# Kernel tuning notes

Hardware: AMD Instinct MI355X
Metric: run time of the kernel (lower is better)

## Reference

```python
import jax, jax.numpy as jnp
import numpy as np

N = 128
NPTS = 120000
G = 64  # voxel grid side


def _build_coords_and_nbrs():
    rng = np.random.default_rng(0)
    lin = rng.choice(G ** 3, size=NPTS, replace=False)
    xs = lin // (G * G)
    ys = (lin // G) % G
    zs = lin % G
    lut = np.full(G ** 3, -1, np.int32)
    lut[lin] = np.arange(NPTS, dtype=np.int32)
    nbr = np.full((NPTS, 27), -1, np.int32)
    k = 0
    for dx in (-1, 0, 1):
        for dy in (-1, 0, 1):
            for dz in (-1, 0, 1):
                nx, ny, nz = xs + dx, ys + dy, zs + dz
                ok = (nx >= 0) & (nx < G) & (ny >= 0) & (ny < G) & (nz >= 0) & (nz < G)
                nl = np.clip(nx * G * G + ny * G + nz, 0, G ** 3 - 1)
                nbr[:, k] = np.where(ok, lut[nl], -1)
                k += 1
    return nbr


def setup_inputs() -> dict:
    key = jax.random.key(0)
    k = jax.random.split(key, 6)
    H = N // 2
    x = jax.random.normal(k[0], (NPTS, N), jnp.float32)
    W1s = jax.random.normal(k[1], (6, N, H), jnp.float32) * np.sqrt(2.0 / N)
    Wks = jax.random.normal(k[2], (6, 27, H, H), jnp.float32) * np.sqrt(2.0 / (27 * H))
    W2s = jax.random.normal(k[3], (6, H, N), jnp.float32) * np.sqrt(1.0 / H)
    Wf = jax.random.normal(k[4], (N, N), jnp.float32) * np.sqrt(1.0 / N)
    nbr_idx = jnp.asarray(_build_coords_and_nbrs())
    return {"x": x, "W1s": W1s, "Wks": Wks, "W2s": W2s, "Wf": Wf, "nbr_idx": nbr_idx}


def reference(x, W1s, Wks, W2s, Wf, nbr_idx):
    valid = nbr_idx >= 0                      # [NPTS, 27]
    safe = jnp.maximum(nbr_idx, 0)

    def conv3(h, Wk):
        # gather-matmul-scatter over the 27 coordinate offsets (as ME does)
        out = jnp.zeros((h.shape[0], Wk.shape[2]), h.dtype)
        for kk in range(27):
            g = jnp.where(valid[:, kk, None], h[safe[:, kk]], 0.0)
            out = out + g @ Wk[kk]
        return out

    def residual_unit(h, i):
        t = jax.nn.relu(h @ W1s[i])           # 1x1 conv N -> N/2
        t = jax.nn.relu(conv3(t, Wks[i]))     # 3^3 sparse conv N/2 -> N/2
        t = t @ W2s[i]                        # 1x1 conv N/2 -> N
        return jax.nn.relu(t + h)

    a = x
    for i in range(3):
        a = residual_unit(a, i)
    b = x
    for i in range(3, 6):
        b = residual_unit(b, i)
    b = b @ Wf                                # final 1x1 conv in branch b
    return a * jax.nn.sigmoid(b) + x
```

## Files before the change

### kernel.cpp

```cpp
#include <hip/hip_runtime.h>
#include <stdint.h>

#define NPTS 120000

typedef __attribute__((ext_vector_type(8))) short bf16x8;
typedef __attribute__((ext_vector_type(4))) float f32x4;

__device__ __forceinline__ uint16_t f2b(float f) {
    union { float f; uint32_t i; } v; v.f = f;
    uint32_t x = v.i;
    return (uint16_t)((x + 0x7fffu + ((x >> 16) & 1u)) >> 16);
}
__device__ __forceinline__ float b2f(uint16_t u) {
    union { uint32_t i; float f; } v; v.i = ((uint32_t)u) << 16; return v.f;
}
__device__ __forceinline__ bf16x8 cvt8(f32x4 a, f32x4 b) {
    bf16x8 t;
    t[0] = (short)f2b(a[0]); t[1] = (short)f2b(a[1]);
    t[2] = (short)f2b(a[2]); t[3] = (short)f2b(a[3]);
    t[4] = (short)f2b(b[0]); t[5] = (short)f2b(b[1]);
    t[6] = (short)f2b(b[2]); t[7] = (short)f2b(b[3]);
    return t;
}
#define MFMA(a, b, c) __builtin_amdgcn_mfma_f32_16x16x32_bf16((a), (b), (c), 0, 0, 0)

__global__ __launch_bounds__(256) void k_swz(
    const float* __restrict__ W1s, const float* __restrict__ Wks,
    const float* __restrict__ W2s, const float* __restrict__ Wf,
    uint16_t* __restrict__ Z, uint16_t* __restrict__ T1z)
{
    if (blockIdx.x == 0 && threadIdx.x < 64)
        T1z[(size_t)NPTS * 64 + threadIdx.x] = 0;
    int idx = blockIdx.x * 256 + threadIdx.x;
    if (idx >= 778240) return;
    const float* src; int K, N, r;
    if (idx < 49152)       { src = W1s + (idx / 8192) * 8192;           K = 128; N = 64;  r = idx & 8191; }
    else if (idx < 712704) { int t = idx - 49152;  src = Wks + (t >> 12) * 4096; K = 64;  N = 64;  r = t & 4095; }
    else if (idx < 761856) { int t = idx - 712704; src = W2s + (t / 8192) * 8192; K = 64;  N = 128; r = t & 8191; }
    else                   { src = Wf; K = 128; N = 128; r = idx - 761856; }
    int j  = r & 7;
    int l  = (r >> 3) & 63;
    int t2 = r >> 9;
    int KC = K >> 5;
    int kc = t2 % KC;
    int nt = t2 / KC;
    int k  = kc * 32 + (l >> 4) * 8 + j;
    int n  = nt * 16 + (l & 15);
    Z[idx] = f2b(src[k * N + n]);
}

__global__ __launch_bounds__(256) void k_gemm1(
    const float* __restrict__ H, const uint16_t* __restrict__ Wz,
    uint16_t* __restrict__ T)
{
    const int tid = threadIdx.x;
    const int wv = tid >> 6, ln = tid & 63;
    const int m = ln & 15, part = ln >> 4;
    const long rb = (long)blockIdx.x * 64 + wv * 16;

    bf16x8 a[4];
    const float* hrow = H + (rb + m) * 128 + part * 8;
    #pragma unroll
    for (int kc = 0; kc < 4; ++kc) {
        f32x4 h0 = *reinterpret_cast<const f32x4*>(hrow + kc * 32);
        f32x4 h1 = *reinterpret_cast<const f32x4*>(hrow + kc * 32 + 4);
        a[kc] = cvt8(h0, h1);
    }
    #pragma unroll
    for (int nt = 0; nt < 4; ++nt) {
        f32x4 acc = (f32x4)(0.0f);
        #pragma unroll
        for (int kc = 0; kc < 4; ++kc) {
            bf16x8 b = *reinterpret_cast<const bf16x8*>(Wz + ((nt * 4 + kc) * 64 + ln) * 8);
            acc = MFMA(a[kc], b, acc);
        }
        #pragma unroll
        for (int r = 0; r < 4; ++r) {
            float v = acc[r] > 0.f ? acc[r] : 0.f;
            T[(rb + part * 4 + r) * 64 + nt * 16 + m] = f2b(v);
        }
    }
}

__global__ __launch_bounds__(256) void k_convg2(
    const uint16_t* __restrict__ T,
    const uint16_t* __restrict__ Wkz,
    const uint16_t* __restrict__ W2z,
    const float* Hin,
    const int* __restrict__ nbr,
    float* HoutF, uint16_t* __restrict__ HoutB, int out_bf16)
{
    __shared__ int snbr[27 * 48];
    __shared__ __align__(16) float red[3 * 3072];
    __shared__ __align__(16) uint16_t sc2[48 * 72];
    const int tid = threadIdx.x;
    const int wv = tid >> 6, ln = tid & 63;
    const int mrow = ln & 15, part = ln >> 4;
    const long bb = (long)blockIdx.x * 48;

    for (int i = tid; i < 1296; i += 256) {
        int lp = i / 27, kk = i - lp * 27;
        int n = nbr[(bb + lp) * 27 + kk];
        snbr[kk * 48 + lp] = (n < 0) ? NPTS : n;
    }
    __syncthreads();

    f32x4 acc[3][4];
    #pragma unroll
    for (int mm = 0; mm < 3; ++mm)
        #pragma unroll
        for (int nt = 0; nt < 4; ++nt) acc[mm][nt] = (f32x4)(0.0f);

    for (int k = wv; k < 27; k += 4) {
        bf16x8 A[3][2];
        #pragma unroll
        for (int mm = 0; mm < 3; ++mm) {
            long r0 = (long)snbr[k * 48 + mm * 16 + mrow] * 64;
            A[mm][0] = *reinterpret_cast<const bf16x8*>(T + r0 + part * 8);
            A[mm][1] = *reinterpret_cast<const bf16x8*>(T + r0 + 32 + part * 8);
        }
        const uint16_t* wb = Wkz + k * 4096;
        bf16x8 B[8];
        #pragma unroll
        for (int i = 0; i < 8; ++i)
            B[i] = *reinterpret_cast<const bf16x8*>(wb + (i * 64 + ln) * 8);
        #pragma unroll
        for (int nt = 0; nt < 4; ++nt)
            #pragma unroll
            for (int mm = 0; mm < 3; ++mm) {
                acc[mm][nt] = MFMA(A[mm][0], B[nt * 2 + 0], acc[mm][nt]);
                acc[mm][nt] = MFMA(A[mm][1], B[nt * 2 + 1], acc[mm][nt]);
            }
    }

    if (wv > 0) {
        float* buf = &red[(wv - 1) * 3072];
        #pragma unroll
        for (int mm = 0; mm < 3; ++mm)
            #pragma unroll
            for (int nt = 0; nt < 4; ++nt)
                #pragma unroll
                for (int r = 0; r < 4; ++r)
                    buf[(mm * 16 + part * 4 + r) * 64 + nt * 16 + mrow] = acc[mm][nt][r];
    }
    __syncthreads();
    if (wv == 0) {
        #pragma unroll
        for (int mm = 0; mm < 3; ++mm)
            #pragma unroll
            for (int nt = 0; nt < 4; ++nt)
                #pragma unroll
                for (int r = 0; r < 4; ++r) {
                    int idx = (mm * 16 + part * 4 + r) * 64 + nt * 16 + mrow;
                    float v = acc[mm][nt][r] + red[idx] + red[3072 + idx] + red[6144 + idx];
                    v = v > 0.f ? v : 0.f;
                    sc2[(mm * 16 + part * 4 + r) * 72 + nt * 16 + mrow] = f2b(v);
                }
    }
    __syncthreads();

    bf16x8 a2[3][2];
    #pragma unroll
    for (int mm = 0; mm < 3; ++mm) {
        const uint16_t* crow = sc2 + (mm * 16 + mrow) * 72;
        a2[mm][0] = *reinterpret_cast<const bf16x8*>(crow + part * 8);
        a2[mm][1] = *reinterpret_cast<const bf16x8*>(crow + 32 + part * 8);
    }
    f32x4 acc2[3][2];
    #pragma unroll
    for (int mm = 0; mm < 3; ++mm)
        #pragma unroll
        for (int j = 0; j < 2; ++j) acc2[mm][j] = (f32x4)(0.0f);
    #pragma unroll
    for (int j = 0; j < 2; ++j) {
        int nt = wv * 2 + j;
        bf16x8 b0 = *reinterpret_cast<const bf16x8*>(W2z + ((nt * 2 + 0) * 64 + ln) * 8);
        bf16x8 b1 = *reinterpret_cast<const bf16x8*>(W2z + ((nt * 2 + 1) * 64 + ln) * 8);
        #pragma unroll
        for (int mm = 0; mm < 3; ++mm) {
            acc2[mm][j] = MFMA(a2[mm][0], b0, acc2[mm][j]);
            acc2[mm][j] = MFMA(a2[mm][1], b1, acc2[mm][j]);
        }
    }
    if (out_bf16) {
        #pragma unroll
        for (int mm = 0; mm < 3; ++mm)
            #pragma unroll
            for (int j = 0; j < 2; ++j)
                #pragma unroll
                for (int r = 0; r < 4; ++r) {
                    long p = bb + mm * 16 + part * 4 + r;
                    int col = (wv * 2 + j) * 16 + mrow;
                    float v = acc2[mm][j][r] + Hin[p * 128 + col];
                    v = v > 0.f ? v : 0.f;
                    HoutB[p * 128 + col] = f2b(v);
                }
    } else {
        #pragma unroll
        for (int mm = 0; mm < 3; ++mm)
            #pragma unroll
            for (int j = 0; j < 2; ++j)
                #pragma unroll
                for (int r = 0; r < 4; ++r) {
                    long p = bb + mm * 16 + part * 4 + r;
                    int col = (wv * 2 + j) * 16 + mrow;
                    float v = acc2[mm][j][r] + Hin[p * 128 + col];
                    HoutF[p * 128 + col] = v > 0.f ? v : 0.f;
                }
    }
}

__global__ __launch_bounds__(256) void k_final(
    const float* B, const uint16_t* __restrict__ Wfz,
    const uint16_t* __restrict__ A16, const float* __restrict__ X,
    float* Out)
{
    const int tid = threadIdx.x;
    const int wv = tid >> 6, ln = tid & 63;
    const int m = ln & 15, part = ln >> 4;
    const long rb = (long)blockIdx.x * 64 + wv * 16;

    bf16x8 a[4];
    const float* brow = B + (rb + m) * 128 + part * 8;
    #pragma unroll
    for (int kc = 0; kc < 4; ++kc) {
        f32x4 h0 = *reinterpret_cast<const f32x4*>(brow + kc * 32);
        f32x4 h1 = *reinterpret_cast<const f32x4*>(brow + kc * 32 + 4);
        a[kc] = cvt8(h0, h1);
    }
    #pragma unroll
    for (int nt = 0; nt < 8; ++nt) {
        f32x4 acc = (f32x4)(0.0f);
        #pragma unroll
        for (int kc = 0; kc < 4; ++kc) {
            bf16x8 b = *reinterpret_cast<const bf16x8*>(Wfz + ((nt * 4 + kc) * 64 + ln) * 8);
            acc = MFMA(a[kc], b, acc);
        }
        #pragma unroll
        for (int r = 0; r < 4; ++r) {
            long p = rb + part * 4 + r;
            int col = nt * 16 + m;
            float s = 1.f / (1.f + __expf(-acc[r]));
            float av = b2f(A16[p * 128 + col]);
            Out[p * 128 + col] = av * s + X[p * 128 + col];
        }
    }
}

extern "C" void kernel_launch(void* const* d_in, const int* in_sizes, int n_in,
                              void* d_out, int out_size, void* d_ws, size_t ws_size,
                              hipStream_t stream)
{
    const float* x   = (const float*)d_in[0];
    const float* W1s = (const float*)d_in[1];
    const float* Wks = (const float*)d_in[2];
    const float* W2s = (const float*)d_in[3];
    const float* Wf  = (const float*)d_in[4];
    const int*   nbr = (const int*)d_in[5];
    float*       out = (float*)d_out;

    uint16_t* A16 = (uint16_t*)d_ws;
    uint16_t* T1  = A16 + (size_t)NPTS * 128;
    uint16_t* Z   = T1 + (size_t)(NPTS + 1) * 64;
    const uint16_t* W1z = Z;
    const uint16_t* Wkz = Z + 49152;
    const uint16_t* W2z = Z + 712704;
    const uint16_t* Wfz = Z + 761856;

    k_swz<<<dim3(3040), dim3(256), 0, stream>>>(W1s, Wks, W2s, Wf, Z, T1);

    auto unit = [&](int i, const float* hin, float* houtF, uint16_t* houtB, int obf) {
        k_gemm1<<<dim3(1875), dim3(256), 0, stream>>>(hin, W1z + (size_t)i * 8192, T1);
        k_convg2<<<dim3(2500), dim3(256), 0, stream>>>(T1, Wkz + (size_t)i * 110592,
                                                       W2z + (size_t)i * 8192,
                                                       hin, nbr, houtF, houtB, obf);
    };

    unit(0, x,   out, nullptr, 0);
    unit(1, out, out, nullptr, 0);
    unit(2, out, out, A16,     1);
    unit(3, x,   out, nullptr, 0);
    unit(4, out, out, nullptr, 0);
    unit(5, out, out, nullptr, 0);
    k_final<<<dim3(1875), dim3(256), 0, stream>>>(out, Wfz, A16, x, out);
}
```

Baseline: 739.4 us.

## Run sparse conv block as single wave with double-buffered neighbor gathers

The gather-conv-plus-1x1 kernel drops from four waves per 48-point block, each handling a subset of taps, to a single wave that processes all 27 taps. This removes the cross-wave LDS reduction and the block barriers. Gathered rows are double-buffered so the load for the next tap overlaps the MFMAs of the current one, and the neighbor table is stored in its original layout. In exchange, each block does four times as much serial work with a quarter of the threads, so latency hiding now depends on running many small blocks per CU.

After: 795.2 us. 1.08x slower.

```diff
diff --git a/kernel.cpp b/kernel.cpp
--- a/kernel.cpp
+++ b/kernel.cpp
@@ -82,7 +82,7 @@
     }
 }
 
-__global__ __launch_bounds__(256) void k_convg2(
+__global__ __launch_bounds__(64) void k_convg2(
     const uint16_t* __restrict__ T,
     const uint16_t* __restrict__ Wkz,
     const uint16_t* __restrict__ W2z,
@@ -90,20 +90,19 @@
     const int* __restrict__ nbr,
     float* HoutF, uint16_t* __restrict__ HoutB, int out_bf16)
 {
-    __shared__ int snbr[27 * 48];
-    __shared__ __align__(16) float red[3 * 3072];
-    __shared__ __align__(16) uint16_t sc2[48 * 72];
-    const int tid = threadIdx.x;
-    const int wv = tid >> 6, ln = tid & 63;
+    __shared__ int snbr[48 * 27];
+    __shared__ __align__(16) uint16_t sc2[48 * 80];
+    const int ln = threadIdx.x;
     const int mrow = ln & 15, part = ln >> 4;
+    const int pc8 = part * 8;
     const long bb = (long)blockIdx.x * 48;
 
-    for (int i = tid; i < 1296; i += 256) {
-        int lp = i / 27, kk = i - lp * 27;
-        int n = nbr[(bb + lp) * 27 + kk];
-        snbr[kk * 48 + lp] = (n < 0) ? NPTS : n;
-    }
-    __syncthreads();
+    const int* nb = nbr + bb * 27;
+    for (int i = ln; i < 1296; i += 64) {
+        int n = nb[i];
+        snbr[i] = (n < 0) ? NPTS : n;
+    }
+    __builtin_amdgcn_wave_barrier();
 
     f32x4 acc[3][4];
     #pragma unroll
@@ -111,102 +110,99 @@
         #pragma unroll
         for (int nt = 0; nt < 4; ++nt) acc[mm][nt] = (f32x4)(0.0f);
 
-    for (int k = wv; k < 27; k += 4) {
-        bf16x8 A[3][2];
-        #pragma unroll
-        for (int mm = 0; mm < 3; ++mm) {
-            long r0 = (long)snbr[k * 48 + mm * 16 + mrow] * 64;
-            A[mm][0] = *reinterpret_cast<const bf16x8*>(T + r0 + part * 8);
-            A[mm][1] = *reinterpret_cast<const bf16x8*>(T + r0 + 32 + part * 8);
-        }
-        const uint16_t* wb = Wkz + k * 4096;
-        bf16x8 B[8];
-        #pragma unroll
-        for (int i = 0; i < 8; ++i)
-            B[i] = *reinterpret_cast<const bf16x8*>(wb + (i * 64 + ln) * 8);
+    bf16x8 Aa[3][2], Ab[3][2];
+
+#define LOADA(Adst, kk)                                                         \
+    {                                                                           \
+        _Pragma("unroll")                                                       \
+        for (int mm = 0; mm < 3; ++mm) {                                        \
+            long r0 = (long)snbr[(mm * 16 + mrow) * 27 + (kk)] << 6;            \
+            Adst[mm][0] = *reinterpret_cast<const bf16x8*>(T + r0 + pc8);       \
+            Adst[mm][1] = *reinterpret_cast<const bf16x8*>(T + r0 + 32 + pc8);  \
+        }                                                                       \
+    }
+
+#define TAP(Asrc, kk)                                                           \
+    {                                                                           \
+        const uint16_t* wb = Wkz + (kk) * 4096;                                 \
+        bf16x8 B[8];                                                            \
+        _Pragma("unroll")                                                       \
+        for (int i = 0; i < 8; ++i)                                             \
+            B[i] = *reinterpret_cast<const bf16x8*>(wb + (i * 64 + ln) * 8);    \
+        _Pragma("unroll")                                                       \
+        for (int nt = 0; nt < 4; ++nt) {                                        \
+            _Pragma("unroll")                                                   \
+            for (int mm = 0; mm < 3; ++mm) {                                    \
+                acc[mm][nt] = MFMA(Asrc[mm][0], B[nt * 2 + 0], acc[mm][nt]);    \
+                acc[mm][nt] = MFMA(Asrc[mm][1], B[nt * 2 + 1], acc[mm][nt]);    \
+            }                                                                   \
+        }                                                                       \
+    }
+
+    LOADA(Aa, 0);
+    #pragma unroll 1
+    for (int k = 0; k < 26; k += 2) {
+        LOADA(Ab, k + 1);
+        TAP(Aa, k);
+        LOADA(Aa, k + 2);
+        TAP(Ab, k + 1);
+    }
+    TAP(Aa, 26);
+#undef LOADA
+#undef TAP
+
+    #pragma unroll
+    for (int mm = 0; mm < 3; ++mm)
         #pragma unroll
         for (int nt = 0; nt < 4; ++nt)
             #pragma unroll
-            for (int mm = 0; mm < 3; ++mm) {
-                acc[mm][nt] = MFMA(A[mm][0], B[nt * 2 + 0], acc[mm][nt]);
-                acc[mm][nt] = MFMA(A[mm][1], B[nt * 2 + 1], acc[mm][nt]);
+            for (int r = 0; r < 4; ++r) {
+                float v = acc[mm][nt][r];
+                v = v > 0.f ? v : 0.f;
+                sc2[(mm * 16 + part * 4 + r) * 80 + nt * 16 + mrow] = f2b(v);
             }
-    }
-
-    if (wv > 0) {
-        float* buf = &red[(wv - 1) * 3072];
-        #pragma unroll
-        for (int mm = 0; mm < 3; ++mm)
-            #pragma unroll
-            for (int nt = 0; nt < 4; ++nt)
-                #pragma unroll
-                for (int r = 0; r < 4; ++r)
-                    buf[(mm * 16 + part * 4 + r) * 64 + nt * 16 + mrow] = acc[mm][nt][r];
-    }
-    __syncthreads();
-    if (wv == 0) {
-        #pragma unroll
-        for (int mm = 0; mm < 3; ++mm)
-            #pragma unroll
-            for (int nt = 0; nt < 4; ++nt)
-                #pragma unroll
-                for (int r = 0; r < 4; ++r) {
-                    int idx = (mm * 16 + part * 4 + r) * 64 + nt * 16 + mrow;
-                    float v = acc[mm][nt][r] + red[idx] + red[3072 + idx] + red[6144 + idx];
-                    v = v > 0.f ? v : 0.f;
-                    sc2[(mm * 16 + part * 4 + r) * 72 + nt * 16 + mrow] = f2b(v);
-                }
-    }
-    __syncthreads();
+    __builtin_amdgcn_wave_barrier();
 
     bf16x8 a2[3][2];
     #pragma unroll
     for (int mm = 0; mm < 3; ++mm) {
-        const uint16_t* crow = sc2 + (mm * 16 + mrow) * 72;
-        a2[mm][0] = *reinterpret_cast<const bf16x8*>(crow + part * 8);
-        a2[mm][1] = *reinterpret_cast<const bf16x8*>(crow + 32 + part * 8);
-    }
-    f32x4 acc2[3][2];
-    #pragma unroll
-    for (int mm = 0; mm < 3; ++mm)
-        #pragma unroll
-        for (int j = 0; j < 2; ++j) acc2[mm][j] = (f32x4)(0.0f);
-    #pragma unroll
-    for (int j = 0; j < 2; ++j) {
-        int nt = wv * 2 + j;
+        const uint16_t* crow = sc2 + (mm * 16 + mrow) * 80;
+        a2[mm][0] = *reinterpret_cast<const bf16x8*>(crow + pc8);
+        a2[mm][1] = *reinterpret_cast<const bf16x8*>(crow + 32 + pc8);
+    }
+
+    #pragma unroll 2
+    for (int nt = 0; nt < 8; ++nt) {
         bf16x8 b0 = *reinterpret_cast<const bf16x8*>(W2z + ((nt * 2 + 0) * 64 + ln) * 8);
         bf16x8 b1 = *reinterpret_cast<const bf16x8*>(W2z + ((nt * 2 + 1) * 64 + ln) * 8);
+        f32x4 c[3];
         #pragma unroll
         for (int mm = 0; mm < 3; ++mm) {
-            acc2[mm][j] = MFMA(a2[mm][0], b0, acc2[mm][j]);
-            acc2[mm][j] = MFMA(a2[mm][1], b1, acc2[mm][j]);
-        }
-    }
-    if (out_bf16) {
-        #pragma unroll
-        for (int mm = 0; mm < 3; ++mm)
+            c[mm] = (f32x4)(0.0f);
+            c[mm] = MFMA(a2[mm][0], b0, c[mm]);
+            c[mm] = MFMA(a2[mm][1], b1, c[mm]);
+        }
+        const int col = nt * 16 + mrow;
+        if (out_bf16) {
             #pragma unroll
-            for (int j = 0; j < 2; ++j)
+            for (int mm = 0; mm < 3; ++mm)
                 #pragma unroll
                 for (int r = 0; r < 4; ++r) {
                     long p = bb + mm * 16 + part * 4 + r;
-                    int col = (wv * 2 + j) * 16 + mrow;
-                    float v = acc2[mm][j][r] + Hin[p * 128 + col];
+                    float v = c[mm][r] + Hin[p * 128 + col];
                     v = v > 0.f ? v : 0.f;
                     HoutB[p * 128 + col] = f2b(v);
                 }
-    } else {
-        #pragma unroll
-        for (int mm = 0; mm < 3; ++mm)
+        } else {
             #pragma unroll
-            for (int j = 0; j < 2; ++j)
+            for (int mm = 0; mm < 3; ++mm)
                 #pragma unroll
                 for (int r = 0; r < 4; ++r) {
                     long p = bb + mm * 16 + part * 4 + r;
-                    int col = (wv * 2 + j) * 16 + mrow;
-                    float v = acc2[mm][j][r] + Hin[p * 128 + col];
+                    float v = c[mm][r] + Hin[p * 128 + col];
                     HoutF[p * 128 + col] = v > 0.f ? v : 0.f;
                 }
+        }
     }
 }
 
@@ -271,9 +267,9 @@
 
     auto unit = [&](int i, const float* hin, float* houtF, uint16_t* houtB, int obf) {
         k_gemm1<<<dim3(1875), dim3(256), 0, stream>>>(hin, W1z + (size_t)i * 8192, T1);
-        k_convg2<<<dim3(2500), dim3(256), 0, stream>>>(T1, Wkz + (size_t)i * 110592,
-                                                       W2z + (size_t)i * 8192,
-                                                       hin, nbr, houtF, houtB, obf);
+        k_convg2<<<dim3(2500), dim3(64), 0, stream>>>(T1, Wkz + (size_t)i * 110592,
+                                                      W2z + (size_t)i * 8192,
+                                                      hin, nbr, houtF, houtB, obf);
     };
 
     unit(0, x,   out, nullptr, 0);
```

## Fuse next unit's 1x1 conv and final gating into sparse conv epilogue

Applied to the files above, without the earlier changes.

The conv kernel's epilogue now computes the next residual unit's first 1x1 conv (N→N/2 with ReLU) from the freshly produced rows, held in shared memory as bf16. Its output goes to a second ping-pong T buffer. The last unit's epilogue also does the final Wf matmul, the sigmoid gating and the residual add, so the separate gemm1 and final kernels are no longer launched. This removes several full passes that re-read the fp32 activations, at the cost of more workspace, extra register and shared-memory pressure in the conv kernel, and a fallback path when the workspace is too small.

Result: no change. 731.3 us (-1.1%).

```diff
diff --git a/kernel.cpp b/kernel.cpp
--- a/kernel.cpp
+++ b/kernel.cpp
@@ -27,10 +27,15 @@
 __global__ __launch_bounds__(256) void k_swz(
     const float* __restrict__ W1s, const float* __restrict__ Wks,
     const float* __restrict__ W2s, const float* __restrict__ Wf,
-    uint16_t* __restrict__ Z, uint16_t* __restrict__ T1z)
+    uint16_t* __restrict__ Z, uint16_t* __restrict__ T1z,
+    uint16_t* __restrict__ T2z)
 {
-    if (blockIdx.x == 0 && threadIdx.x < 64)
-        T1z[(size_t)NPTS * 64 + threadIdx.x] = 0;
+    if (blockIdx.x == 0) {
+        if (threadIdx.x < 64)
+            T1z[(size_t)NPTS * 64 + threadIdx.x] = 0;
+        else if (threadIdx.x < 128 && T2z)
+            T2z[(size_t)NPTS * 64 + (threadIdx.x - 64)] = 0;
+    }
     int idx = blockIdx.x * 256 + threadIdx.x;
     if (idx >= 778240) return;
     const float* src; int K, N, r;
@@ -88,7 +93,14 @@
     const uint16_t* __restrict__ W2z,
     const float* Hin,
     const int* __restrict__ nbr,
-    float* HoutF, uint16_t* __restrict__ HoutB, int out_bf16)
+    float* HoutF,
+    uint16_t* __restrict__ HoutB,
+    const uint16_t* __restrict__ Wn,
+    uint16_t* __restrict__ Tn,
+    const float* __restrict__ Xg,
+    const uint16_t* __restrict__ A16g,
+    float* __restrict__ OutF,
+    int mode)
 {
     __shared__ int snbr[27 * 48];
     __shared__ __align__(16) float red[3 * 3072];
@@ -182,7 +194,46 @@
             acc2[mm][j] = MFMA(a2[mm][1], b1, acc2[mm][j]);
         }
     }
-    if (out_bf16) {
+
+    uint16_t* sH = (uint16_t*)red;
+
+    if (mode == 0) {
+        #pragma unroll
+        for (int mm = 0; mm < 3; ++mm)
+            #pragma unroll
+            for (int j = 0; j < 2; ++j)
+                #pragma unroll
+                for (int r = 0; r < 4; ++r) {
+                    int lr = mm * 16 + part * 4 + r;
+                    long p = bb + lr;
+                    int col = (wv * 2 + j) * 16 + mrow;
+                    float v = acc2[mm][j][r] + Hin[p * 128 + col];
+                    v = v > 0.f ? v : 0.f;
+                    HoutF[p * 128 + col] = v;
+                    sH[lr * 136 + col] = f2b(v);
+                }
+        if (Tn) {
+            __syncthreads();
+            f32x4 t1a[3] = { (f32x4)(0.f), (f32x4)(0.f), (f32x4)(0.f) };
+            #pragma unroll
+            for (int kc = 0; kc < 4; ++kc) {
+                bf16x8 b = *reinterpret_cast<const bf16x8*>(Wn + ((wv * 4 + kc) * 64 + ln) * 8);
+                #pragma unroll
+                for (int mm = 0; mm < 3; ++mm) {
+                    bf16x8 a = *reinterpret_cast<const bf16x8*>(
+                        sH + (mm * 16 + mrow) * 136 + kc * 32 + part * 8);
+                    t1a[mm] = MFMA(a, b, t1a[mm]);
+                }
+            }
+            #pragma unroll
+            for (int mm = 0; mm < 3; ++mm)
+                #pragma unroll
+                for (int r = 0; r < 4; ++r) {
+                    float v = t1a[mm][r]; v = v > 0.f ? v : 0.f;
+                    Tn[(bb + mm * 16 + part * 4 + r) * 64 + wv * 16 + mrow] = f2b(v);
+                }
+        }
+    } else if (mode == 1) {
         #pragma unroll
         for (int mm = 0; mm < 3; ++mm)
             #pragma unroll
@@ -195,6 +246,27 @@
                     v = v > 0.f ? v : 0.f;
                     HoutB[p * 128 + col] = f2b(v);
                 }
+        if (Tn) {
+            f32x4 t1a[3] = { (f32x4)(0.f), (f32x4)(0.f), (f32x4)(0.f) };
+            #pragma unroll
+            for (int kc = 0; kc < 4; ++kc) {
+                bf16x8 b = *reinterpret_cast<const bf16x8*>(Wn + ((wv * 4 + kc) * 64 + ln) * 8);
+                #pragma unroll
+                for (int mm = 0; mm < 3; ++mm) {
+                    const float* xr = Xg + (bb + mm * 16 + mrow) * 128 + kc * 32 + part * 8;
+                    f32x4 h0 = *reinterpret_cast<const f32x4*>(xr);
+                    f32x4 h1 = *reinterpret_cast<const f32x4*>(xr + 4);
+                    t1a[mm] = MFMA(cvt8(h0, h1), b, t1a[mm]);
+                }
+            }
+            #pragma unroll
+            for (int mm = 0; mm < 3; ++mm)
+                #pragma unroll
+                for (int r = 0; r < 4; ++r) {
+                    float v = t1a[mm][r]; v = v > 0.f ? v : 0.f;
+                    Tn[(bb + mm * 16 + part * 4 + r) * 64 + wv * 16 + mrow] = f2b(v);
+                }
+        }
     } else {
         #pragma unroll
         for (int mm = 0; mm < 3; ++mm)
@@ -202,11 +274,42 @@
             for (int j = 0; j < 2; ++j)
                 #pragma unroll
                 for (int r = 0; r < 4; ++r) {
-                    long p = bb + mm * 16 + part * 4 + r;
+                    int lr = mm * 16 + part * 4 + r;
+                    long p = bb + lr;
                     int col = (wv * 2 + j) * 16 + mrow;
                     float v = acc2[mm][j][r] + Hin[p * 128 + col];
-                    HoutF[p * 128 + col] = v > 0.f ? v : 0.f;
-                }
+                    v = v > 0.f ? v : 0.f;
+                    sH[lr * 136 + col] = f2b(v);
+                }
+        __syncthreads();
+        bf16x8 af[3][4];
+        #pragma unroll
+        for (int mm = 0; mm < 3; ++mm)
+            #pragma unroll
+            for (int kc = 0; kc < 4; ++kc)
+                af[mm][kc] = *reinterpret_cast<const bf16x8*>(
+                    sH + (mm * 16 + mrow) * 136 + kc * 32 + part * 8);
+        #pragma unroll
+        for (int j = 0; j < 2; ++j) {
+            int nt = wv * 2 + j;
+            f32x4 fa[3] = { (f32x4)(0.f), (f32x4)(0.f), (f32x4)(0.f) };
+            #pragma unroll
+            for (int kc = 0; kc < 4; ++kc) {
+                bf16x8 b = *reinterpret_cast<const bf16x8*>(Wn + ((nt * 4 + kc) * 64 + ln) * 8);
+                #pragma unroll
+                for (int mm = 0; mm < 3; ++mm)
+                    fa[mm] = MFMA(af[mm][kc], b, fa[mm]);
+            }
+            #pragma unroll
+            for (int mm = 0; mm < 3; ++mm)
+                #pragma unroll
+                for (int r = 0; r < 4; ++r) {
+                    long p = bb + mm * 16 + part * 4 + r;
+                    int col = nt * 16 + mrow;
+                    float s = 1.f / (1.f + __expf(-fa[mm][r]));
+                    OutF[p * 128 + col] = b2f(A16g[p * 128 + col]) * s + Xg[p * 128 + col];
+                }
+        }
     }
 }
 
@@ -259,28 +362,52 @@
     const int*   nbr = (const int*)d_in[5];
     float*       out = (float*)d_out;
 
+    const size_t A16_n = (size_t)NPTS * 128;
+    const size_t T_n   = (size_t)(NPTS + 1) * 64;
+    const size_t Z_n   = 778240;
+    const size_t need2 = (A16_n + 2 * T_n + Z_n) * 2;
+
     uint16_t* A16 = (uint16_t*)d_ws;
-    uint16_t* T1  = A16 + (size_t)NPTS * 128;
-    uint16_t* Z   = T1 + (size_t)(NPTS + 1) * 64;
+    uint16_t* Ta  = A16 + A16_n;
+    bool dual = ws_size >= need2;
+    uint16_t* Tb  = dual ? Ta + T_n : nullptr;
+    uint16_t* Z   = dual ? Tb + T_n : Ta + T_n;
     const uint16_t* W1z = Z;
     const uint16_t* Wkz = Z + 49152;
     const uint16_t* W2z = Z + 712704;
     const uint16_t* Wfz = Z + 761856;
 
-    k_swz<<<dim3(3040), dim3(256), 0, stream>>>(W1s, Wks, W2s, Wf, Z, T1);
-
-    auto unit = [&](int i, const float* hin, float* houtF, uint16_t* houtB, int obf) {
-        k_gemm1<<<dim3(1875), dim3(256), 0, stream>>>(hin, W1z + (size_t)i * 8192, T1);
-        k_convg2<<<dim3(2500), dim3(256), 0, stream>>>(T1, Wkz + (size_t)i * 110592,
-                                                       W2z + (size_t)i * 8192,
-                                                       hin, nbr, houtF, houtB, obf);
-    };
-
-    unit(0, x,   out, nullptr, 0);
-    unit(1, out, out, nullptr, 0);
-    unit(2, out, out, A16,     1);
-    unit(3, x,   out, nullptr, 0);
-    unit(4, out, out, nullptr, 0);
-    unit(5, out, out, nullptr, 0);
-    k_final<<<dim3(1875), dim3(256), 0, stream>>>(out, Wfz, A16, x, out);
-}
+    k_swz<<<dim3(3040), dim3(256), 0, stream>>>(W1s, Wks, W2s, Wf, Z, Ta, Tb);
+
+    if (dual) {
+        auto conv = [&](int i, const uint16_t* Tc, const float* hin,
+                        float* houtF, uint16_t* houtB,
+                        const uint16_t* wn, uint16_t* tn,
+                        const float* xg, const uint16_t* a16g, float* outF, int mode) {
+            k_convg2<<<dim3(2500), dim3(256), 0, stream>>>(
+                Tc, Wkz + (size_t)i * 110592, W2z + (size_t)i * 8192,
+                hin, nbr, houtF, houtB, wn, tn, xg, a16g, outF, mode);
+        };
+        k_gemm1<<<dim3(1875), dim3(256), 0, stream>>>(x, W1z, Ta);
+        conv(0, Ta, x,   out, nullptr, W1z + 1 * 8192, Tb, nullptr, nullptr, nullptr, 0);
+        conv(1, Tb, out, out, nullptr, W1z + 2 * 8192, Ta, nullptr, nullptr, nullptr, 0);
+        conv(2, Ta, out, nullptr, A16, W1z + 3 * 8192, Tb, x,       nullptr, nullptr, 1);
+        conv(3, Tb, x,   out, nullptr, W1z + 4 * 8192, Ta, nullptr, nullptr, nullptr, 0);
+        conv(4, Ta, out, out, nullptr, W1z + 5 * 8192, Tb, nullptr, nullptr, nullptr, 0);
+        conv(5, Tb, out, nullptr, nullptr, Wfz, nullptr, x, A16, out, 2);
+    } else {
+        auto unit = [&](int i, const float* hin, float* houtF, uint16_t* houtB, int m) {
+            k_gemm1<<<dim3(1875), dim3(256), 0, stream>>>(hin, W1z + (size_t)i * 8192, Ta);
+            k_convg2<<<dim3(2500), dim3(256), 0, stream>>>(
+                Ta, Wkz + (size_t)i * 110592, W2z + (size_t)i * 8192,
+                hin, nbr, houtF, houtB, nullptr, nullptr, nullptr, nullptr, nullptr, m);
+        };
+        unit(0, x,   out, nullptr, 0);
+        unit(1, out, out, nullptr, 0);
+        unit(2, out, nullptr, A16, 1);
+        unit(3, x,   out, nullptr, 0);
+        unit(4, out, out, nullptr, 0);
+        unit(5, out, out, nullptr, 0);
+        k_final<<<dim3(1875), dim3(256), 0, stream>>>(out, Wfz, A16, x, out);
+    }
+}
```

## Restructure sparse conv: per-wave point tiles, LDS double-buffered weights, fused final GEMM

Applied to the files above, without the earlier changes.

The conv kernel now gives each wave its own 48 points and has it loop over all 27 offsets, instead of splitting offsets across waves. This removes the cross-wave LDS reduction. Each offset's weight slice is staged cooperatively into a double-buffered LDS tile, and a pre-transposed neighbour index table (pre-shifted into row offsets) is prefetched one offset ahead. The final Wf GEMM with sigmoid gating is fused into the last conv launch, which removes k_final and one full read of the fp32 intermediate. In exchange there is a block-wide sync on every offset, a larger block with fewer blocks, and a one-time transpose kernel for the neighbour table.

New measurement: 675.5 us. 1.09x faster.

```diff
diff --git a/kernel.cpp b/kernel.cpp
--- a/kernel.cpp
+++ b/kernel.cpp
@@ -49,6 +49,24 @@
     Z[idx] = f2b(src[k * N + n]);
 }
 
+__global__ __launch_bounds__(256) void k_nbrT(
+    const int* __restrict__ nbr, int* __restrict__ nbrT)
+{
+    __shared__ int st[27 * 64];
+    const int tid = threadIdx.x;
+    const long p0 = (long)blockIdx.x * 64;
+    for (int i = tid; i < 1728; i += 256) {
+        int lp = i / 27, kk = i - lp * 27;
+        int n = nbr[p0 * 27 + i];
+        st[kk * 64 + lp] = ((n < 0) ? NPTS : n) << 6;
+    }
+    __syncthreads();
+    for (int i = tid; i < 1728; i += 256) {
+        int kk = i >> 6, lp = i & 63;
+        nbrT[(long)kk * NPTS + p0 + lp] = st[i];
+    }
+}
+
 __global__ __launch_bounds__(256) void k_gemm1(
     const float* __restrict__ H, const uint16_t* __restrict__ Wz,
     uint16_t* __restrict__ T)
@@ -82,27 +100,39 @@
     }
 }
 
-__global__ __launch_bounds__(256) void k_convg2(
+template<int MODE>
+__global__ __launch_bounds__(256, (MODE == 2) ? 2 : 3) void k_conv(
     const uint16_t* __restrict__ T,
     const uint16_t* __restrict__ Wkz,
     const uint16_t* __restrict__ W2z,
     const float* Hin,
-    const int* __restrict__ nbr,
-    float* HoutF, uint16_t* __restrict__ HoutB, int out_bf16)
-{
-    __shared__ int snbr[27 * 48];
-    __shared__ __align__(16) float red[3 * 3072];
-    __shared__ __align__(16) uint16_t sc2[48 * 72];
+    const int* __restrict__ nbrT,
+    float* HoutF,
+    uint16_t* __restrict__ HoutB,
+    const uint16_t* __restrict__ Wfz,
+    const uint16_t* __restrict__ A16g,
+    const float* __restrict__ Xg,
+    float* __restrict__ OutF)
+{
+    constexpr int SLICE_SH = (MODE == 2) ? 6528 : 3456;
+    __shared__ __align__(16) uint16_t wkbuf[2][4096];
+    __shared__ __align__(16) uint16_t uni[4][SLICE_SH];
     const int tid = threadIdx.x;
     const int wv = tid >> 6, ln = tid & 63;
-    const int mrow = ln & 15, part = ln >> 4;
-    const long bb = (long)blockIdx.x * 48;
-
-    for (int i = tid; i < 1296; i += 256) {
-        int lp = i / 27, kk = i - lp * 27;
-        int n = nbr[(bb + lp) * 27 + kk];
-        snbr[kk * 48 + lp] = (n < 0) ? NPTS : n;
-    }
+    const int mrow = ln & 15, part = ln >> 4, pc8 = part * 8;
+    const long bb = (long)blockIdx.x * 192;
+    const long wb0 = bb + wv * 48;
+
+    {
+        const uint16_t* g = Wkz + wv * 1024 + ln * 8;
+        bf16x8 s0 = *reinterpret_cast<const bf16x8*>(g);
+        bf16x8 s1 = *reinterpret_cast<const bf16x8*>(g + 512);
+        *reinterpret_cast<bf16x8*>(&wkbuf[0][wv * 1024 + ln * 8]) = s0;
+        *reinterpret_cast<bf16x8*>(&wkbuf[0][wv * 1024 + 512 + ln * 8]) = s1;
+    }
+    int idx[3];
+    #pragma unroll
+    for (int mm = 0; mm < 3; ++mm) idx[mm] = nbrT[wb0 + mm * 16 + mrow];
     __syncthreads();
 
     f32x4 acc[3][4];
@@ -111,19 +141,29 @@
         #pragma unroll
         for (int nt = 0; nt < 4; ++nt) acc[mm][nt] = (f32x4)(0.0f);
 
-    for (int k = wv; k < 27; k += 4) {
+    int cur = 0;
+    #pragma unroll 1
+    for (int k = 0; k < 27; ++k) {
         bf16x8 A[3][2];
         #pragma unroll
         for (int mm = 0; mm < 3; ++mm) {
-            long r0 = (long)snbr[k * 48 + mm * 16 + mrow] * 64;
-            A[mm][0] = *reinterpret_cast<const bf16x8*>(T + r0 + part * 8);
-            A[mm][1] = *reinterpret_cast<const bf16x8*>(T + r0 + 32 + part * 8);
-        }
-        const uint16_t* wb = Wkz + k * 4096;
+            const uint16_t* s = T + (long)idx[mm] + pc8;
+            A[mm][0] = *reinterpret_cast<const bf16x8*>(s);
+            A[mm][1] = *reinterpret_cast<const bf16x8*>(s + 32);
+        }
+        bf16x8 s0, s1;
+        if (k < 26) {
+            const uint16_t* g = Wkz + (k + 1) * 4096 + wv * 1024 + ln * 8;
+            s0 = *reinterpret_cast<const bf16x8*>(g);
+            s1 = *reinterpret_cast<const bf16x8*>(g + 512);
+            const int* ib = nbrT + (long)(k + 1) * NPTS + wb0;
+            #pragma unroll
+            for (int mm = 0; mm < 3; ++mm) idx[mm] = ib[mm * 16 + mrow];
+        }
         bf16x8 B[8];
         #pragma unroll
         for (int i = 0; i < 8; ++i)
-            B[i] = *reinterpret_cast<const bf16x8*>(wb + (i * 64 + ln) * 8);
+            B[i] = *reinterpret_cast<const bf16x8*>(&wkbuf[cur][i * 512 + ln * 8]);
         #pragma unroll
         for (int nt = 0; nt < 4; ++nt)
             #pragma unroll
@@ -131,118 +171,110 @@
                 acc[mm][nt] = MFMA(A[mm][0], B[nt * 2 + 0], acc[mm][nt]);
                 acc[mm][nt] = MFMA(A[mm][1], B[nt * 2 + 1], acc[mm][nt]);
             }
-    }
-
-    if (wv > 0) {
-        float* buf = &red[(wv - 1) * 3072];
-        #pragma unroll
-        for (int mm = 0; mm < 3; ++mm)
-            #pragma unroll
-            for (int nt = 0; nt < 4; ++nt)
-                #pragma unroll
-                for (int r = 0; r < 4; ++r)
-                    buf[(mm * 16 + part * 4 + r) * 64 + nt * 16 + mrow] = acc[mm][nt][r];
-    }
-    __syncthreads();
-    if (wv == 0) {
-        #pragma unroll
-        for (int mm = 0; mm < 3; ++mm)
-            #pragma unroll
-            for (int nt = 0; nt < 4; ++nt)
-                #pragma unroll
-                for (int r = 0; r < 4; ++r) {
-                    int idx = (mm * 16 + part * 4 + r) * 64 + nt * 16 + mrow;
-                    float v = acc[mm][nt][r] + red[idx] + red[3072 + idx] + red[6144 + idx];
-                    v = v > 0.f ? v : 0.f;
-                    sc2[(mm * 16 + part * 4 + r) * 72 + nt * 16 + mrow] = f2b(v);
-                }
-    }
-    __syncthreads();
+        if (k < 26) {
+            *reinterpret_cast<bf16x8*>(&wkbuf[cur ^ 1][wv * 1024 + ln * 8]) = s0;
+            *reinterpret_cast<bf16x8*>(&wkbuf[cur ^ 1][wv * 1024 + 512 + ln * 8]) = s1;
+        }
+        __syncthreads();
+        cur ^= 1;
+    }
+
+    uint16_t* sc2 = &uni[wv][0];
+    #pragma unroll
+    for (int mm = 0; mm < 3; ++mm)
+        #pragma unroll
+        for (int nt = 0; nt < 4; ++nt)
+            #pragma unroll
+            for (int r = 0; r < 4; ++r) {
+                float v = acc[mm][nt][r];
+                v = v > 0.f ? v : 0.f;
+                sc2[(mm * 16 + part * 4 + r) * 72 + nt * 16 + mrow] = f2b(v);
+            }
+    __builtin_amdgcn_wave_barrier();
 
     bf16x8 a2[3][2];
     #pragma unroll
     for (int mm = 0; mm < 3; ++mm) {
         const uint16_t* crow = sc2 + (mm * 16 + mrow) * 72;
-        a2[mm][0] = *reinterpret_cast<const bf16x8*>(crow + part * 8);
-        a2[mm][1] = *reinterpret_cast<const bf16x8*>(crow + 32 + part * 8);
-    }
-    f32x4 acc2[3][2];
-    #pragma unroll
-    for (int mm = 0; mm < 3; ++mm)
-        #pragma unroll
-        for (int j = 0; j < 2; ++j) acc2[mm][j] = (f32x4)(0.0f);
-    #pragma unroll
-    for (int j = 0; j < 2; ++j) {
-        int nt = wv * 2 + j;
+        a2[mm][0] = *reinterpret_cast<const bf16x8*>(crow + pc8);
+        a2[mm][1] = *reinterpret_cast<const bf16x8*>(crow + 32 + pc8);
+    }
+    __builtin_amdgcn_wave_barrier();
+
+    #pragma unroll 2
+    for (int nt = 0; nt < 8; ++nt) {
         bf16x8 b0 = *reinterpret_cast<const bf16x8*>(W2z + ((nt * 2 + 0) * 64 + ln) * 8);
         bf16x8 b1 = *reinterpret_cast<const bf16x8*>(W2z + ((nt * 2 + 1) * 64 + ln) * 8);
+        f32x4 c[3];
         #pragma unroll
         for (int mm = 0; mm < 3; ++mm) {
-            acc2[mm][j] = MFMA(a2[mm][0], b0, acc2[mm][j]);
-            acc2[mm][j] = MFMA(a2[mm][1], b1, acc2[mm][j]);
-        }
-    }
-    if (out_bf16) {
-        #pragma unroll
-        for (int mm = 0; mm < 3; ++mm)
-            #pragma unroll
-            for (int j = 0; j < 2; ++j)
+            c[mm] = (f32x4)(0.0f);
+            c[mm] = MFMA(a2[mm][0], b0, c[mm]);
+            c[mm] = MFMA(a2[mm][1], b1, c[mm]);
+        }
+        const int col = nt * 16 + mrow;
+        if (MODE == 0) {
+            #pragma unroll
+            for (int mm = 0; mm < 3; ++mm)
                 #pragma unroll
                 for (int r = 0; r < 4; ++r) {
-                    long p = bb + mm * 16 + part * 4 + r;
-                    int col = (wv * 2 + j) * 16 + mrow;
-                    float v = acc2[mm][j][r] + Hin[p * 128 + col];
+                    long p = wb0 + mm * 16 + part * 4 + r;
+                    float v = c[mm][r] + Hin[p * 128 + col];
+                    HoutF[p * 128 + col] = v > 0.f ? v : 0.f;
+                }
+        } else if (MODE == 1) {
+            #pragma unroll
+            for (int mm = 0; mm < 3; ++mm)
+                #pragma unroll
+                for (int r = 0; r < 4; ++r) {
+                    long p = wb0 + mm * 16 + part * 4 + r;
+                    float v = c[mm][r] + Hin[p * 128 + col];
                     v = v > 0.f ? v : 0.f;
                     HoutB[p * 128 + col] = f2b(v);
                 }
-    } else {
+        } else {
+            uint16_t* sH = &uni[wv][0];
+            #pragma unroll
+            for (int mm = 0; mm < 3; ++mm)
+                #pragma unroll
+                for (int r = 0; r < 4; ++r) {
+                    long p = wb0 + mm * 16 + part * 4 + r;
+                    float v = c[mm][r] + Hin[p * 128 + col];
+                    v = v > 0.f ? v : 0.f;
+                    sH[(mm * 16 + part * 4 + r) * 136 + col] = f2b(v);
+                }
+        }
+    }
+
+    if (MODE == 2) {
+        __builtin_amdgcn_wave_barrier();
+        const uint16_t* sH = &uni[wv][0];
+        bf16x8 af[3][4];
         #pragma unroll
         for (int mm = 0; mm < 3; ++mm)
             #pragma unroll
-            for (int j = 0; j < 2; ++j)
+            for (int kc = 0; kc < 4; ++kc)
+                af[mm][kc] = *reinterpret_cast<const bf16x8*>(
+                    sH + (mm * 16 + mrow) * 136 + kc * 32 + pc8);
+        #pragma unroll 2
+        for (int nt = 0; nt < 8; ++nt) {
+            f32x4 fa[3] = { (f32x4)(0.f), (f32x4)(0.f), (f32x4)(0.f) };
+            #pragma unroll
+            for (int kc = 0; kc < 4; ++kc) {
+                bf16x8 b = *reinterpret_cast<const bf16x8*>(Wfz + ((nt * 4 + kc) * 64 + ln) * 8);
+                #pragma unroll
+                for (int mm = 0; mm < 3; ++mm)
+                    fa[mm] = MFMA(af[mm][kc], b, fa[mm]);
+            }
+            const int col = nt * 16 + mrow;
+            #pragma unroll
+            for (int mm = 0; mm < 3; ++mm)
                 #pragma unroll
                 for (int r = 0; r < 4; ++r) {
-                    long p = bb + mm * 16 + part * 4 + r;
-                    int col = (wv * 2 + j) * 16 + mrow;
-                    float v = acc2[mm][j][r] + Hin[p * 128 + col];
-                    HoutF[p * 128 + col] = v > 0.f ? v : 0.f;
+                    long p = wb0 + mm * 16 + part * 4 + r;
+                    float s = 1.f / (1.f + __expf(-fa[mm][r]));
+                    OutF[p * 128 + col] = b2f(A16g[p * 128 + col]) * s + Xg[p * 128 + col];
                 }
-    }
-}
-
-__global__ __launch_bounds__(256) void k_final(
-    const float* B, const uint16_t* __restrict__ Wfz,
-    const uint16_t* __restrict__ A16, const float* __restrict__ X,
-    float* Out)
-{
-    const int tid = threadIdx.x;
-    const int wv = tid >> 6, ln = tid & 63;
-    const int m = ln & 15, part = ln >> 4;
-    const long rb = (long)blockIdx.x * 64 + wv * 16;
-
-    bf16x8 a[4];
-    const float* brow = B + (rb + m) * 128 + part * 8;
-    #pragma unroll
-    for (int kc = 0; kc < 4; ++kc) {
-        f32x4 h0 = *reinterpret_cast<const f32x4*>(brow + kc * 32);
-        f32x4 h1 = *reinterpret_cast<const f32x4*>(brow + kc * 32 + 4);
-        a[kc] = cvt8(h0, h1);
-    }
-    #pragma unroll
-    for (int nt = 0; nt < 8; ++nt) {
-        f32x4 acc = (f32x4)(0.0f);
-        #pragma unroll
-        for (int kc = 0; kc < 4; ++kc) {
-            bf16x8 b = *reinterpret_cast<const bf16x8*>(Wfz + ((nt * 4 + kc) * 64 + ln) * 8);
-            acc = MFMA(a[kc], b, acc);
-        }
-        #pragma unroll
-        for (int r = 0; r < 4; ++r) {
-            long p = rb + part * 4 + r;
-            int col = nt * 16 + m;
-            float s = 1.f / (1.f + __expf(-acc[r]));
-            float av = b2f(A16[p * 128 + col]);
-            Out[p * 128 + col] = av * s + X[p * 128 + col];
         }
     }
 }
@@ -262,25 +294,35 @@
     uint16_t* A16 = (uint16_t*)d_ws;
     uint16_t* T1  = A16 + (size_t)NPTS * 128;
     uint16_t* Z   = T1 + (size_t)(NPTS + 1) * 64;
+    int* nbrT     = (int*)(Z + 778240);
     const uint16_t* W1z = Z;
     const uint16_t* Wkz = Z + 49152;
     const uint16_t* W2z = Z + 712704;
     const uint16_t* Wfz = Z + 761856;
 
-    k_swz<<<dim3(3040), dim3(256), 0, stream>>>(W1s, Wks, W2s, Wf, Z, T1);
-
-    auto unit = [&](int i, const float* hin, float* houtF, uint16_t* houtB, int obf) {
-        k_gemm1<<<dim3(1875), dim3(256), 0, stream>>>(hin, W1z + (size_t)i * 8192, T1);
-        k_convg2<<<dim3(2500), dim3(256), 0, stream>>>(T1, Wkz + (size_t)i * 110592,
-                                                       W2z + (size_t)i * 8192,
-                                                       hin, nbr, houtF, houtB, obf);
+    k_swz <<<dim3(3040), dim3(256), 0, stream>>>(W1s, Wks, W2s, Wf, Z, T1);
+    k_nbrT<<<dim3(1875), dim3(256), 0, stream>>>(nbr, nbrT);
+
+    auto g1 = [&](int i, const float* h) {
+        k_gemm1<<<dim3(1875), dim3(256), 0, stream>>>(h, W1z + (size_t)i * 8192, T1);
     };
 
-    unit(0, x,   out, nullptr, 0);
-    unit(1, out, out, nullptr, 0);
-    unit(2, out, out, A16,     1);
-    unit(3, x,   out, nullptr, 0);
-    unit(4, out, out, nullptr, 0);
-    unit(5, out, out, nullptr, 0);
-    k_final<<<dim3(1875), dim3(256), 0, stream>>>(out, Wfz, A16, x, out);
-}
+    g1(0, x);
+    k_conv<0><<<dim3(625), dim3(256), 0, stream>>>(T1, Wkz + 0 * 110592, W2z + 0 * 8192,
+        x,   nbrT, out, nullptr, nullptr, nullptr, nullptr, nullptr);
+    g1(1, out);
+    k_conv<0><<<dim3(625), dim3(256), 0, stream>>>(T1, Wkz + 1 * 110592, W2z + 1 * 8192,
+        out, nbrT, out, nullptr, nullptr, nullptr, nullptr, nullptr);
+    g1(2, out);
+    k_conv<1><<<dim3(625), dim3(256), 0, stream>>>(T1, Wkz + 2 * 110592, W2z + 2 * 8192,
+        out, nbrT, nullptr, A16, nullptr, nullptr, nullptr, nullptr);
+    g1(3, x);
+    k_conv<0><<<dim3(625), dim3(256), 0, stream>>>(T1, Wkz + 3 * 110592, W2z + 3 * 8192,
+        x,   nbrT, out, nullptr, nullptr, nullptr, nullptr, nullptr);
+    g1(4, out);
+    k_conv<0><<<dim3(625), dim3(256), 0, stream>>>(T1, Wkz + 4 * 110592, W2z + 4 * 8192,
+        out, nbrT, out, nullptr, nullptr, nullptr, nullptr, nullptr);
+    g1(5, out);
+    k_conv<2><<<dim3(625), dim3(256), 0, stream>>>(T1, Wkz + 5 * 110592, W2z + 5 * 8192,
+        out, nbrT, nullptr, nullptr, Wfz, A16, x, out);
+}
```
